# Kernel optimization log

Hardware: AMD Instinct MI355X
Metric: run time of the kernel (lower is better)

Reference implementation:

```python
import jax, jax.numpy as jnp
import numpy as np

N_NODES = 50000
N_EDGES = 800000
EMB = 128
N_LAYERS = 2
BN_EPS = 1e-5


def setup_inputs() -> dict:
    key = jax.random.key(0)
    ks = jax.random.split(key, 16)
    N, E, D, L = N_NODES, N_EDGES, EMB, N_LAYERS
    x = jax.random.randint(ks[0], (N, 2), 0, 3)
    edge_index = jax.random.randint(ks[1], (2, E), 0, N)
    edge_attr = jax.random.randint(ks[2], (E, 2), 0, 3)
    batch = jnp.zeros((N,), dtype=jnp.int32)
    s = 0.1
    xemb1 = jax.random.normal(ks[3], (120, D)) * s   # atom-type embedding
    xemb2 = jax.random.normal(ks[4], (3, D)) * s     # chirality embedding
    e1 = jax.random.normal(ks[5], (L, 7, D)) * s     # bond-type embedding per layer
    e2 = jax.random.normal(ks[6], (L, 3, D)) * s     # bond-direction embedding per layer
    W1 = jax.random.normal(ks[7], (L, D, 2 * D)) * s
    b1 = jnp.zeros((L, 2 * D))
    W2 = jax.random.normal(ks[8], (L, 2 * D, D)) * s
    b2 = jnp.zeros((L, D))
    gamma = jnp.ones((L, D))
    beta = jnp.zeros((L, D))
    return {"x": x, "edge_index": edge_index, "edge_attr": edge_attr, "batch": batch,
            "xemb1": xemb1, "xemb2": xemb2, "e1": e1, "e2": e2,
            "W1": W1, "b1": b1, "W2": W2, "b2": b2, "gamma": gamma, "beta": beta}


def _gnn_forward(x, edge_index, edge_attr, xemb1, xemb2, e1, e2, W1, b1, W2, b2, gamma, beta):
    N = x.shape[0]
    # add self loops; self-loop edge_attr = [4, 0]
    loop = jnp.arange(N, dtype=edge_index.dtype)
    src = jnp.concatenate([edge_index[0], loop])
    dst = jnp.concatenate([edge_index[1], loop])
    loop_attr = jnp.concatenate([jnp.full((N, 1), 4, dtype=edge_attr.dtype),
                                 jnp.zeros((N, 1), dtype=edge_attr.dtype)], axis=1)
    ea = jnp.concatenate([edge_attr, loop_attr], axis=0)  # [E+N, 2]

    # input node embedding
    h = xemb1[x[:, 0]] + xemb2[x[:, 1]]  # [N, D]

    for l in range(N_LAYERS):
        eemb = e1[l][ea[:, 0]] + e2[l][ea[:, 1]]      # [E+N, D]
        msg = h[src] + eemb                            # gather + edge fuse
        agg = jax.ops.segment_sum(msg, dst, num_segments=N)  # scatter-add
        # GIN update MLP: Linear -> ReLU -> Linear
        h2 = jax.nn.relu(agg @ W1[l] + b1[l]) @ W2[l] + b2[l]
        # BatchNorm1d (training mode: biased batch stats)
        mu = jnp.mean(h2, axis=0)
        var = jnp.mean(jnp.square(h2 - mu), axis=0)
        h2 = gamma[l] * (h2 - mu) * jax.lax.rsqrt(var + BN_EPS) + beta[l]
        # dropout(relu) for non-final layers; drop_ratio=0 -> identity dropout
        h = h2 if l == N_LAYERS - 1 else jax.nn.relu(h2)
    return h  # JK='last'


def reference(x, edge_index, edge_attr, batch, xemb1, xemb2, e1, e2, W1, b1, W2, b2, gamma, beta):
    return _gnn_forward(x, edge_index, edge_attr, xemb1, xemb2, e1, e2, W1, b1, W2, b2, gamma, beta)
```

## Files before the change

### kernel.cpp

```cpp
#include <hip/hip_runtime.h>
#include <stdint.h>

#define N_NODES 50000
#define N_EDGES 800000
#define EMB 128
#define NPAD 50176
#define BN_EPS 1e-5f
#define SENT_KEY ((N_NODES << 5) | 21)
#define NODES_PER_XCD 6250
#define XCHUNK 2048
#define NCHUNKS ((N_EDGES + XCHUNK - 1) / XCHUNK)
#define PBLK 196

typedef __attribute__((ext_vector_type(8))) short short8;
typedef __attribute__((ext_vector_type(4))) float f32x4;

__device__ __forceinline__ unsigned short f2bf(float f) {
    unsigned int u = __float_as_uint(f);
    u += 0x7fffu + ((u >> 16) & 1u);
    return (unsigned short)(u >> 16);
}
__device__ __forceinline__ float bflo(unsigned int v) { return __uint_as_float(v << 16); }
__device__ __forceinline__ float bfhi(unsigned int v) { return __uint_as_float(v & 0xffff0000u); }
__device__ __forceinline__ unsigned int packbf(float lo, float hi) {
    return (unsigned int)f2bf(lo) | ((unsigned int)f2bf(hi) << 16);
}

__global__ void k_prep(const int* __restrict__ x, const float* __restrict__ xe1,
                       const float* __restrict__ xe2, unsigned int* __restrict__ h,
                       const float* __restrict__ W1, const float* __restrict__ W2,
                       unsigned short* __restrict__ w1t, unsigned short* __restrict__ w2t,
                       int* __restrict__ deg,
                       const int* __restrict__ ei, const int* __restrict__ ea,
                       int* __restrict__ keyv) {
    int idx = blockIdx.x * 256 + threadIdx.x;
    int i = idx >> 6, j = idx & 63;
    if (i < N_NODES) {
        int a = x[2 * i], c = x[2 * i + 1];
        float2 va = *(const float2*)(xe1 + a * EMB + j * 2);
        float2 vb = *(const float2*)(xe2 + c * EMB + j * 2);
        h[i * 64 + j] = packbf(va.x + vb.x, va.y + vb.y);
    } else if (i == N_NODES) {
        h[(size_t)i * 64 + j] = 0u;
    }
    if (idx < 4 * 32768) {
        int sec = idx >> 15, q = idx & 32767;
        if (sec < 2) {
            int r = q >> 8, c = q & 255;
            w1t[sec * 32768 + c * 128 + r] = f2bf(W1[sec * 32768 + q]);
        } else {
            int s = sec - 2;
            int r = q >> 7, c = q & 127;
            w2t[s * 32768 + c * 256 + r] = f2bf(W2[s * 32768 + q]);
        }
    }
    if (idx < N_EDGES) {
        int2 aa = *(const int2*)(ea + 2 * idx);
        keyv[idx] = (ei[idx] << 5) | (aa.x * 3 + aa.y);
        atomicAdd(&deg[ei[N_EDGES + idx]], 1);
    }
}

__global__ void k_alloc(const int* __restrict__ deg, int* __restrict__ gcur,
                        int* __restrict__ offs, int* __restrict__ cursor,
                        int* __restrict__ keys, int* __restrict__ bcnt,
                        const float* __restrict__ e1, const float* __restrict__ e2,
                        const float* __restrict__ W1, unsigned short* __restrict__ w1e) {
    __shared__ int wbase[4];
    __shared__ int lc[8];
    int tid = threadIdx.x, lane = tid & 63, wid = tid >> 6;
    if (tid < 8) lc[tid] = 0;
    int i = blockIdx.x * 256 + tid;
    int d = (i < N_NODES) ? deg[i] : 0;
    int pd = (d + 15) & ~15;
    int s = pd;
#pragma unroll
    for (int off = 1; off < 64; off <<= 1) {
        int t = __shfl_up(s, off);
        if (lane >= off) s += t;
    }
    if (lane == 63) wbase[wid] = s;
    __syncthreads();
    if (tid == 0) {
        int t0 = wbase[0], t1 = wbase[1], t2 = wbase[2], t3 = wbase[3];
        int b = atomicAdd(gcur, t0 + t1 + t2 + t3);
        wbase[0] = b; wbase[1] = b + t0; wbase[2] = b + t0 + t1; wbase[3] = b + t0 + t1 + t2;
    }
    __syncthreads();
    if (i < N_NODES) {
        int o = wbase[wid] + s - pd;
        offs[i] = o;
        cursor[i] = o;
        for (int j = d; j < pd; ++j) keys[o + j] = SENT_KEY;
        int nch = pd >> 4;
        atomicAdd(&lc[nch > 7 ? 7 : nch], 1);
    }
    __syncthreads();
    if (tid < 8) atomicAdd(&bcnt[tid], lc[tid]);

    if (blockIdx.x < 42) {
        int l = blockIdx.x / 21, c = blockIdx.x % 21;
        int a0 = c / 3, a1 = c - a0 * 3;
        const float* E1 = e1 + l * 896 + a0 * 128;
        const float* E2 = e2 + l * 384 + a1 * 128;
        const float* w1 = W1 + l * 32768;
        int n = tid;
        float acc = 0.f;
        for (int k = 0; k < 128; ++k)
            acc = fmaf(E1[k] + E2[k], w1[k * 256 + n], acc);
        w1e[(size_t)l * 8192 + n * 32 + c] = f2bf(acc);
        if (c == 0) {
            for (int cc = 21; cc < 32; ++cc) w1e[(size_t)l * 8192 + n * 32 + cc] = 0;
        }
    }
}

__global__ void k_fill(const int* __restrict__ dst, const int* __restrict__ keyv,
                       int* __restrict__ cursor, int* __restrict__ keys,
                       const int* __restrict__ deg, const int* __restrict__ bcnt,
                       int* __restrict__ bcur, int* __restrict__ perm) {
    int xcd = blockIdx.x & 7, chunk = blockIdx.x >> 3;
    int lo = xcd * NODES_PER_XCD, hi = lo + NODES_PER_XCD;
    int e0 = chunk * XCHUNK + threadIdx.x * 4;
#pragma unroll
    for (int it = 0; it < XCHUNK / 1024; ++it) {
        int e = e0 + it * 1024;
        if (e < N_EDGES) {
            int4 d4 = *(const int4*)(dst + e);
            int dv[4] = {d4.x, d4.y, d4.z, d4.w};
#pragma unroll
            for (int q = 0; q < 4; ++q) {
                int d = dv[q];
                if (d >= lo && d < hi) {
                    int p = atomicAdd(&cursor[d], 1);
                    keys[p] = keyv[e + q];
                }
            }
        }
    }
    if (blockIdx.x < PBLK) {
        __shared__ int lcnt[8], gbase[8], tbase[8];
        if (threadIdx.x < 8) lcnt[threadIdx.x] = 0;
        __syncthreads();
        int i = blockIdx.x * 256 + threadIdx.x;
        int b = 0, lrank = 0;
        if (i < N_NODES) {
            int nch = (deg[i] + 15) >> 4;
            b = nch > 7 ? 7 : nch;
            lrank = atomicAdd(&lcnt[b], 1);
        }
        __syncthreads();
        if (threadIdx.x < 8) {
            gbase[threadIdx.x] = atomicAdd(&bcur[threadIdx.x], lcnt[threadIdx.x]);
            int s = 0;
            for (int k = 0; k < threadIdx.x; ++k) s += bcnt[k];
            tbase[threadIdx.x] = s;
        }
        __syncthreads();
        if (i < N_NODES) perm[tbase[b] + gbase[b] + lrank] = i;
    }
}

__global__ __launch_bounds__(256) void k_cnt(const int* __restrict__ deg,
                                             const int* __restrict__ offs,
                                             const int* __restrict__ keys,
                                             unsigned int* __restrict__ cntb32) {
    __shared__ int bins[16][24];
    int tid = threadIdx.x, fl = tid & 15, grp = tid >> 4;
    for (int t = tid; t < 16 * 24; t += 256) ((int*)bins)[t] = 0;
    __syncthreads();
    int node = blockIdx.x * 16 + grp;
    int o = 0, pd = 0;
    if (node < N_NODES) { o = offs[node]; pd = (deg[node] + 15) & ~15; }
    for (int j = fl; j < pd; j += 16)
        atomicAdd(&bins[grp][keys[o + j] & 31], 1);
    __syncthreads();
    if (node < NPAD) {
        int c0 = 0, c1 = 0;
        if (node < N_NODES && fl < 11) {
            c0 = bins[grp][2 * fl]     + (fl == 6 ? 1 : 0);
            c1 = bins[grp][2 * fl + 1];
        }
        cntb32[(size_t)node * 16 + fl] = packbf((float)c0, (float)c1);
    }
}

__global__ __launch_bounds__(256, 4) void k_agg(
    const unsigned int* __restrict__ h,
    const int* __restrict__ offs,
    const int* __restrict__ deg,
    const int* __restrict__ keys,
    const int* __restrict__ perm,
    unsigned int* __restrict__ agg)
{
    int wave = threadIdx.x >> 6, lane = threadIdx.x & 63;
    int sub = lane >> 4, fl = lane & 15;
    int wi = blockIdx.x * 4 + wave;
    int q = (wi & 255) * 49 + (wi >> 8);
    int slot = q * 4 + sub;
    int node = (slot < N_NODES) ? perm[slot] : slot;
    float ax[8] = {0.f, 0.f, 0.f, 0.f, 0.f, 0.f, 0.f, 0.f};
    int o = 0, nch = 0;
    if (node < N_NODES) {
        o = offs[node];
        nch = (deg[node] + 15) >> 4;
        uint4 hv = *(const uint4*)(h + (size_t)node * 64 + fl * 4);
        ax[0] = bflo(hv.x);  ax[1] = bfhi(hv.x);
        ax[2] = bflo(hv.y);  ax[3] = bfhi(hv.y);
        ax[4] = bflo(hv.z);  ax[5] = bfhi(hv.z);
        ax[6] = bflo(hv.w);  ax[7] = bfhi(hv.w);
    }
    int maxch = nch;
#pragma unroll
    for (int d = 32; d; d >>= 1) maxch = max(maxch, __shfl_xor(maxch, d));
    int key = (0 < nch) ? keys[o + fl] : SENT_KEY;
    for (int c = 0; c < maxch; ++c) {
        int keyn = (c + 1 < nch) ? keys[o + (c + 1) * 16 + fl] : SENT_KEY;
        uint4 g[8];
#pragma unroll
        for (int j = 0; j < 8; ++j) {
            int kj = __shfl(key, sub * 16 + j);
            g[j] = *(const uint4*)(h + (size_t)(kj >> 5) * 64 + fl * 4);
        }
#pragma unroll
        for (int j = 0; j < 8; ++j) {
            uint4 gg = g[j];
            int kb = __shfl(key, sub * 16 + 8 + j);
            g[j] = *(const uint4*)(h + (size_t)(kb >> 5) * 64 + fl * 4);
            ax[0] += bflo(gg.x);  ax[1] += bfhi(gg.x);
            ax[2] += bflo(gg.y);  ax[3] += bfhi(gg.y);
            ax[4] += bflo(gg.z);  ax[5] += bfhi(gg.z);
            ax[6] += bflo(gg.w);  ax[7] += bfhi(gg.w);
        }
#pragma unroll
        for (int j = 0; j < 8; ++j) {
            uint4 gg = g[j];
            ax[0] += bflo(gg.x);  ax[1] += bfhi(gg.x);
            ax[2] += bflo(gg.y);  ax[3] += bfhi(gg.y);
            ax[4] += bflo(gg.z);  ax[5] += bfhi(gg.z);
            ax[6] += bflo(gg.w);  ax[7] += bfhi(gg.w);
        }
        key = keyn;
    }
    {
        uint4 out;
        out.x = packbf(ax[0], ax[1]); out.y = packbf(ax[2], ax[3]);
        out.z = packbf(ax[4], ax[5]); out.w = packbf(ax[6], ax[7]);
        *(uint4*)(agg + (size_t)node * 64 + fl * 4) = out;
    }
}

__global__ __launch_bounds__(1024, 1) void k_mlp(
    unsigned short* aggh2,
    const unsigned short* __restrict__ cntb,
    const unsigned short* __restrict__ w1t,
    const unsigned short* __restrict__ w1e,
    const float* __restrict__ b1,
    const unsigned short* __restrict__ w2t,
    const float* __restrict__ b2,
    float* __restrict__ bnsum)
{
    __shared__ unsigned short w1s[256 * 128];
    __shared__ unsigned short w2s[128 * 256];
    __shared__ unsigned short w1es[256 * 32];
    __shared__ float bn[256];
    int tid = threadIdx.x;
    int lane = tid & 63;
    int wave = tid >> 6;
    int quad = lane >> 4, r16 = lane & 15;
    int m0 = (blockIdx.x * 16 + wave) * 16;
    int sel  = (lane >> 5) & 1;
    int srcA = ((lane >> 4) & 1) * 32 + r16;
    int srcB = srcA + 16;
    if (tid < 256) bn[tid] = 0.f;

#pragma unroll
    for (int it = 0; it < 9; ++it) {
        int ch = it * 1024 + tid;
        if (ch < 4096) {
            int row = ch >> 4, sl = ch & 15;
            uint4 v = *(const uint4*)(w1t + row * 128 + sl * 8);
            int byte = row * 256 + ((sl * 16) ^ ((row & 7) << 4));
            *(uint4*)((char*)w1s + byte) = v;
        } else if (ch < 8192) {
            int c = ch - 4096;
            int row = c >> 5, sl = c & 31;
            uint4 v = *(const uint4*)(w2t + row * 256 + sl * 8);
            int byte = row * 512 + ((sl * 16) ^ ((row & 7) << 4));
            *(uint4*)((char*)w2s + byte) = v;
        } else {
            int c = ch - 8192;
            int row = c >> 2, sl = c & 3;
            *(uint4*)(w1es + row * 32 + sl * 8) = *(const uint4*)(w1e + row * 32 + sl * 8);
        }
    }

    short8 bagg[5];
#pragma unroll
    for (int c = 0; c < 4; ++c)
        bagg[c] = *(const short8*)(aggh2 + (size_t)(m0 + r16) * 128 + c * 32 + quad * 8);
    bagg[4] = *(const short8*)(cntb + (size_t)(m0 + r16) * 32 + quad * 8);

    float b2v[8];
#pragma unroll
    for (int n = 0; n < 8; ++n) b2v[n] = b2[n * 16 + r16];

    __syncthreads();

    f32x4 acc2[8];
#pragma unroll
    for (int n = 0; n < 8; ++n) acc2[n] = (f32x4){0.f, 0.f, 0.f, 0.f};

    int swz = (r16 & 7) << 4;
    for (int c2 = 0; c2 < 8; ++c2) {
        unsigned int pk[2][2];
#pragma unroll
        for (int ntl = 0; ntl < 2; ++ntl) {
            int nt = c2 * 2 + ntl;
            int row = nt * 16 + r16;
            short8 aw[5];
#pragma unroll
            for (int c = 0; c < 4; ++c)
                aw[c] = *(const short8*)((char*)w1s + row * 256 + ((c * 64 + quad * 16) ^ swz));
            aw[4] = *(const short8*)(w1es + row * 32 + quad * 8);
            float4 bv = *(const float4*)(b1 + nt * 16 + quad * 4);
            f32x4 a1a = {0.f, 0.f, 0.f, 0.f}, a1b = {0.f, 0.f, 0.f, 0.f};
            a1a = __builtin_amdgcn_mfma_f32_16x16x32_bf16(aw[0], bagg[0], a1a, 0, 0, 0);
            a1b = __builtin_amdgcn_mfma_f32_16x16x32_bf16(aw[1], bagg[1], a1b, 0, 0, 0);
            a1a = __builtin_amdgcn_mfma_f32_16x16x32_bf16(aw[2], bagg[2], a1a, 0, 0, 0);
            a1b = __builtin_amdgcn_mfma_f32_16x16x32_bf16(aw[3], bagg[3], a1b, 0, 0, 0);
            a1a = __builtin_amdgcn_mfma_f32_16x16x32_bf16(aw[4], bagg[4], a1a, 0, 0, 0);
            float v0 = a1a[0] + a1b[0] + bv.x; v0 = v0 > 0.f ? v0 : 0.f;
            float v1 = a1a[1] + a1b[1] + bv.y; v1 = v1 > 0.f ? v1 : 0.f;
            float v2 = a1a[2] + a1b[2] + bv.z; v2 = v2 > 0.f ? v2 : 0.f;
            float v3 = a1a[3] + a1b[3] + bv.w; v3 = v3 > 0.f ? v3 : 0.f;
            pk[ntl][0] = packbf(v0, v1);
            pk[ntl][1] = packbf(v2, v3);
        }
        short8 a2f;
        {
            int u0 = __shfl((int)pk[0][0], srcA), w0 = __shfl((int)pk[1][0], srcA);
            int u1 = __shfl((int)pk[0][1], srcA), w1_ = __shfl((int)pk[1][1], srcA);
            int u2 = __shfl((int)pk[0][0], srcB), w2_ = __shfl((int)pk[1][0], srcB);
            int u3 = __shfl((int)pk[0][1], srcB), w3_ = __shfl((int)pk[1][1], srcB);
            union { int i[4]; short8 s; } a2u;
            a2u.i[0] = sel ? w0 : u0;
            a2u.i[1] = sel ? w1_ : u1;
            a2u.i[2] = sel ? w2_ : u2;
            a2u.i[3] = sel ? w3_ : u3;
            a2f = a2u.s;
        }
#pragma unroll
        for (int n = 0; n < 8; ++n) {
            int row = n * 16 + r16;
            short8 bw = *(const short8*)((char*)w2s + row * 512 + ((c2 * 64 + quad * 16) ^ swz));
            acc2[n] = __builtin_amdgcn_mfma_f32_16x16x32_bf16(a2f, bw, acc2[n], 0, 0, 0);
        }
    }
    float s[8], q[8];
#pragma unroll
    for (int n = 0; n < 8; ++n) { s[n] = 0.f; q[n] = 0.f; }
#pragma unroll
    for (int n = 0; n < 8; ++n)
#pragma unroll
        for (int r = 0; r < 4; ++r) {
            int row = m0 + quad * 4 + r;
            float v = acc2[n][r] + b2v[n];
            if (row < N_NODES) {
                aggh2[(size_t)row * 128 + n * 16 + r16] = f2bf(v);
                s[n] += v; q[n] += v * v;
            }
        }
#pragma unroll
    for (int n = 0; n < 8; ++n) {
        s[n] += __shfl_xor(s[n], 16); q[n] += __shfl_xor(q[n], 16);
        s[n] += __shfl_xor(s[n], 32); q[n] += __shfl_xor(q[n], 32);
    }
    if (quad == 0) {
#pragma unroll
        for (int n = 0; n < 8; ++n) {
            atomicAdd(&bn[n * 16 + r16], s[n]);
            atomicAdd(&bn[128 + n * 16 + r16], q[n]);
        }
    }
    __syncthreads();
    if (tid < 256) atomicAdd(&bnsum[tid], bn[tid]);
}

__global__ void k_bnnorm(const uint4* __restrict__ h2, const float* __restrict__ bnsum,
                         const float* __restrict__ gamma, const float* __restrict__ beta,
                         uint4* __restrict__ outb, float4* __restrict__ outf, int mode) {
    __shared__ float ab[256];
    int tid = threadIdx.x;
    if (tid < 128) {
        float mean = bnsum[tid] * (1.f / N_NODES);
        float var  = bnsum[128 + tid] * (1.f / N_NODES) - mean * mean;
        float rstd = rsqrtf(var + BN_EPS);
        float g = gamma[tid];
        ab[tid]       = g * rstd;
        ab[128 + tid] = beta[tid] - mean * g * rstd;
    }
    __syncthreads();
    int idx = blockIdx.x * 256 + tid;
    if (idx >= N_NODES * 16) return;
    int p = (idx & 15) * 8;
    uint4 hv = h2[idx];
    float v0 = bflo(hv.x) * ab[p + 0] + ab[128 + p + 0];
    float v1 = bfhi(hv.x) * ab[p + 1] + ab[128 + p + 1];
    float v2 = bflo(hv.y) * ab[p + 2] + ab[128 + p + 2];
    float v3 = bfhi(hv.y) * ab[p + 3] + ab[128 + p + 3];
    float v4 = bflo(hv.z) * ab[p + 4] + ab[128 + p + 4];
    float v5 = bfhi(hv.z) * ab[p + 5] + ab[128 + p + 5];
    float v6 = bflo(hv.w) * ab[p + 6] + ab[128 + p + 6];
    float v7 = bfhi(hv.w) * ab[p + 7] + ab[128 + p + 7];
    if (mode == 0) {
        v0 = v0 > 0.f ? v0 : 0.f; v1 = v1 > 0.f ? v1 : 0.f;
        v2 = v2 > 0.f ? v2 : 0.f; v3 = v3 > 0.f ? v3 : 0.f;
        v4 = v4 > 0.f ? v4 : 0.f; v5 = v5 > 0.f ? v5 : 0.f;
        v6 = v6 > 0.f ? v6 : 0.f; v7 = v7 > 0.f ? v7 : 0.f;
        uint4 out;
        out.x = packbf(v0, v1); out.y = packbf(v2, v3);
        out.z = packbf(v4, v5); out.w = packbf(v6, v7);
        outb[idx] = out;
    } else {
        outf[2 * idx]     = make_float4(v0, v1, v2, v3);
        outf[2 * idx + 1] = make_float4(v4, v5, v6, v7);
    }
}

extern "C" void kernel_launch(void* const* d_in, const int* in_sizes, int n_in,
                              void* d_out, int out_size, void* d_ws, size_t ws_size,
                              hipStream_t stream) {
    const int* x  = (const int*)d_in[0];
    const int* ei = (const int*)d_in[1];
    const int* ea = (const int*)d_in[2];
    const float* xe1 = (const float*)d_in[4];
    const float* xe2 = (const float*)d_in[5];
    const float* e1  = (const float*)d_in[6];
    const float* e2  = (const float*)d_in[7];
    const float* W1  = (const float*)d_in[8];
    const float* b1  = (const float*)d_in[9];
    const float* W2  = (const float*)d_in[10];
    const float* b2  = (const float*)d_in[11];
    const float* gm  = (const float*)d_in[12];
    const float* bt  = (const float*)d_in[13];

    char* ws = (char*)d_ws;
    size_t off = 0;
    auto take = [&](size_t bytes) -> char* {
        char* p = ws + off;
        off = (off + bytes + 255) & ~(size_t)255;
        return p;
    };
    unsigned int* h_buf = (unsigned int*)take((size_t)(N_NODES + 1) * 64 * 4);
    unsigned int* aggb  = (unsigned int*)take((size_t)NPAD * 64 * 4);
    unsigned short* w1t = (unsigned short*)take((size_t)2 * 32768 * 2);
    unsigned short* w2t = (unsigned short*)take((size_t)2 * 32768 * 2);
    unsigned short* w1e = (unsigned short*)take((size_t)2 * 8192 * 2);
    unsigned int* cntb32 = (unsigned int*)take((size_t)NPAD * 16 * 4);
    int* zbuf   = (int*)take((size_t)(N_NODES + 512 + 32) * 4);
    int* deg    = zbuf;
    float* bnsum = (float*)(zbuf + N_NODES);
    int* bmeta  = zbuf + N_NODES + 512;
    int* offs   = (int*)take((size_t)(N_NODES + 1) * 4);
    int* cursor = (int*)take((size_t)N_NODES * 4);
    int* keys   = (int*)take((size_t)(N_EDGES + N_NODES * 16) * 4);
    int* keyv   = (int*)take((size_t)N_EDGES * 4);
    int* perm   = (int*)take((size_t)N_NODES * 4);
    int* bcnt = bmeta, *bcur = bmeta + 8, *gcur = bmeta + 16;

    hipMemsetAsync(zbuf, 0, (size_t)(N_NODES + 512 + 32) * 4, stream);
    k_prep<<<((N_NODES + 1) * 64 + 255) / 256, 256, 0, stream>>>(x, xe1, xe2, h_buf,
                                                                 W1, W2, w1t, w2t, deg,
                                                                 ei, ea, keyv);
    k_alloc<<<PBLK, 256, 0, stream>>>(deg, gcur, offs, cursor, keys, bcnt,
                                      e1, e2, W1, w1e);
    k_fill<<<8 * NCHUNKS, 256, 0, stream>>>(ei + N_EDGES, keyv, cursor, keys,
                                            deg, bcnt, bcur, perm);
    k_cnt<<<NPAD / 16, 256, 0, stream>>>(deg, offs, keys, cntb32);

    for (int l = 0; l < 2; ++l) {
        k_agg<<<NPAD / 16, 256, 0, stream>>>(h_buf, offs, deg, keys, perm, aggb);
        k_mlp<<<NPAD / 256, 1024, 0, stream>>>((unsigned short*)aggb, (const unsigned short*)cntb32,
                                               w1t + l * 32768, w1e + l * 8192, b1 + l * 256,
                                               w2t + l * 32768, b2 + l * 128, bnsum + l * 256);
        k_bnnorm<<<(N_NODES * 16 + 255) / 256, 256, 0, stream>>>((const uint4*)aggb, bnsum + l * 256,
                                                                 gm + l * 128, bt + l * 128,
                                                                 (uint4*)h_buf, (float4*)d_out, l);
    }
}
```

Measured before the change: 325.9 us.

## Fuse per-layer aggregation, MLP and batchnorm into one cooperative persistent kernel

Replaces the six per-layer launches (gather-aggregate, MLP, batchnorm, for each of two layers) with a single cooperative kernel of 256 blocks of 1024 threads. Grid-wide syncs separate the phases, and each phase loops over its work items. This removes kernel launch gaps and tail effects between the small phases. In exchange, the gather phase now runs with 1024-thread blocks at one block per CU and shares a register budget with the MFMA MLP code, which may cut latency hiding for the irregular loads. It also adds grid-sync overhead.

```diff
diff --git a/kernel.cpp b/kernel.cpp
--- a/kernel.cpp
+++ b/kernel.cpp
@@ -1,5 +1,8 @@
 #include <hip/hip_runtime.h>
+#include <hip/hip_cooperative_groups.h>
 #include <stdint.h>
+
+namespace cg = cooperative_groups;
 
 #define N_NODES 50000
 #define N_EDGES 800000
@@ -185,81 +188,20 @@
     }
 }
 
-__global__ __launch_bounds__(256, 4) void k_agg(
-    const unsigned int* __restrict__ h,
-    const int* __restrict__ offs,
-    const int* __restrict__ deg,
-    const int* __restrict__ keys,
-    const int* __restrict__ perm,
-    unsigned int* __restrict__ agg)
+__global__ __launch_bounds__(1024, 1) void k_layers(
+    unsigned int* h,
+    const int* __restrict__ offs, const int* __restrict__ deg,
+    const int* __restrict__ keys, const int* __restrict__ perm,
+    unsigned int* aggb,
+    const unsigned short* __restrict__ cntb,
+    const unsigned short* __restrict__ w1t_a, const unsigned short* __restrict__ w1e_a,
+    const float* __restrict__ b1_a,
+    const unsigned short* __restrict__ w2t_a, const float* __restrict__ b2_a,
+    float* __restrict__ bnsum_a,
+    const float* __restrict__ gm_a, const float* __restrict__ bt_a,
+    float4* __restrict__ outf)
 {
-    int wave = threadIdx.x >> 6, lane = threadIdx.x & 63;
-    int sub = lane >> 4, fl = lane & 15;
-    int wi = blockIdx.x * 4 + wave;
-    int q = (wi & 255) * 49 + (wi >> 8);
-    int slot = q * 4 + sub;
-    int node = (slot < N_NODES) ? perm[slot] : slot;
-    float ax[8] = {0.f, 0.f, 0.f, 0.f, 0.f, 0.f, 0.f, 0.f};
-    int o = 0, nch = 0;
-    if (node < N_NODES) {
-        o = offs[node];
-        nch = (deg[node] + 15) >> 4;
-        uint4 hv = *(const uint4*)(h + (size_t)node * 64 + fl * 4);
-        ax[0] = bflo(hv.x);  ax[1] = bfhi(hv.x);
-        ax[2] = bflo(hv.y);  ax[3] = bfhi(hv.y);
-        ax[4] = bflo(hv.z);  ax[5] = bfhi(hv.z);
-        ax[6] = bflo(hv.w);  ax[7] = bfhi(hv.w);
-    }
-    int maxch = nch;
-#pragma unroll
-    for (int d = 32; d; d >>= 1) maxch = max(maxch, __shfl_xor(maxch, d));
-    int key = (0 < nch) ? keys[o + fl] : SENT_KEY;
-    for (int c = 0; c < maxch; ++c) {
-        int keyn = (c + 1 < nch) ? keys[o + (c + 1) * 16 + fl] : SENT_KEY;
-        uint4 g[8];
-#pragma unroll
-        for (int j = 0; j < 8; ++j) {
-            int kj = __shfl(key, sub * 16 + j);
-            g[j] = *(const uint4*)(h + (size_t)(kj >> 5) * 64 + fl * 4);
-        }
-#pragma unroll
-        for (int j = 0; j < 8; ++j) {
-            uint4 gg = g[j];
-            int kb = __shfl(key, sub * 16 + 8 + j);
-            g[j] = *(const uint4*)(h + (size_t)(kb >> 5) * 64 + fl * 4);
-            ax[0] += bflo(gg.x);  ax[1] += bfhi(gg.x);
-            ax[2] += bflo(gg.y);  ax[3] += bfhi(gg.y);
-            ax[4] += bflo(gg.z);  ax[5] += bfhi(gg.z);
-            ax[6] += bflo(gg.w);  ax[7] += bfhi(gg.w);
-        }
-#pragma unroll
-        for (int j = 0; j < 8; ++j) {
-            uint4 gg = g[j];
-            ax[0] += bflo(gg.x);  ax[1] += bfhi(gg.x);
-            ax[2] += bflo(gg.y);  ax[3] += bfhi(gg.y);
-            ax[4] += bflo(gg.z);  ax[5] += bfhi(gg.z);
-            ax[6] += bflo(gg.w);  ax[7] += bfhi(gg.w);
-        }
-        key = keyn;
-    }
-    {
-        uint4 out;
-        out.x = packbf(ax[0], ax[1]); out.y = packbf(ax[2], ax[3]);
-        out.z = packbf(ax[4], ax[5]); out.w = packbf(ax[6], ax[7]);
-        *(uint4*)(agg + (size_t)node * 64 + fl * 4) = out;
-    }
-}
-
-__global__ __launch_bounds__(1024, 1) void k_mlp(
-    unsigned short* aggh2,
-    const unsigned short* __restrict__ cntb,
-    const unsigned short* __restrict__ w1t,
-    const unsigned short* __restrict__ w1e,
-    const float* __restrict__ b1,
-    const unsigned short* __restrict__ w2t,
-    const float* __restrict__ b2,
-    float* __restrict__ bnsum)
-{
+    cg::grid_group grid = cg::this_grid();
     __shared__ unsigned short w1s[256 * 128];
     __shared__ unsigned short w2s[128 * 256];
     __shared__ unsigned short w1es[256 * 32];
@@ -268,163 +210,233 @@
     int lane = tid & 63;
     int wave = tid >> 6;
     int quad = lane >> 4, r16 = lane & 15;
-    int m0 = (blockIdx.x * 16 + wave) * 16;
     int sel  = (lane >> 5) & 1;
     int srcA = ((lane >> 4) & 1) * 32 + r16;
     int srcB = srcA + 16;
-    if (tid < 256) bn[tid] = 0.f;
-
-#pragma unroll
-    for (int it = 0; it < 9; ++it) {
-        int ch = it * 1024 + tid;
-        if (ch < 4096) {
-            int row = ch >> 4, sl = ch & 15;
-            uint4 v = *(const uint4*)(w1t + row * 128 + sl * 8);
-            int byte = row * 256 + ((sl * 16) ^ ((row & 7) << 4));
-            *(uint4*)((char*)w1s + byte) = v;
-        } else if (ch < 8192) {
-            int c = ch - 4096;
-            int row = c >> 5, sl = c & 31;
-            uint4 v = *(const uint4*)(w2t + row * 256 + sl * 8);
-            int byte = row * 512 + ((sl * 16) ^ ((row & 7) << 4));
-            *(uint4*)((char*)w2s + byte) = v;
-        } else {
-            int c = ch - 8192;
-            int row = c >> 2, sl = c & 3;
-            *(uint4*)(w1es + row * 32 + sl * 8) = *(const uint4*)(w1e + row * 32 + sl * 8);
-        }
-    }
-
-    short8 bagg[5];
-#pragma unroll
-    for (int c = 0; c < 4; ++c)
-        bagg[c] = *(const short8*)(aggh2 + (size_t)(m0 + r16) * 128 + c * 32 + quad * 8);
-    bagg[4] = *(const short8*)(cntb + (size_t)(m0 + r16) * 32 + quad * 8);
-
-    float b2v[8];
-#pragma unroll
-    for (int n = 0; n < 8; ++n) b2v[n] = b2[n * 16 + r16];
-
-    __syncthreads();
-
-    f32x4 acc2[8];
-#pragma unroll
-    for (int n = 0; n < 8; ++n) acc2[n] = (f32x4){0.f, 0.f, 0.f, 0.f};
-
-    int swz = (r16 & 7) << 4;
-    for (int c2 = 0; c2 < 8; ++c2) {
-        unsigned int pk[2][2];
-#pragma unroll
-        for (int ntl = 0; ntl < 2; ++ntl) {
-            int nt = c2 * 2 + ntl;
-            int row = nt * 16 + r16;
-            short8 aw[5];
+    unsigned short* aggh2 = (unsigned short*)aggb;
+
+    for (int l = 0; l < 2; ++l) {
+        const unsigned short* w1t = w1t_a + l * 32768;
+        const unsigned short* w1e = w1e_a + l * 8192;
+        const float* b1 = b1_a + l * 256;
+        const unsigned short* w2t = w2t_a + l * 32768;
+        const float* b2 = b2_a + l * 128;
+        float* bnsum = bnsum_a + l * 256;
+
+        {
+            int rw = blockIdx.x * 16 + wave;
+            for (int it = 0; it < 4; ++it) {
+                int wi = it * 4096 + rw;
+                if (wi >= 12544) break;
+                int q = (wi & 255) * 49 + (wi >> 8);
+                int slot = q * 4 + quad;
+                int node = (slot < N_NODES) ? perm[slot] : slot;
+                float ax[8] = {0.f, 0.f, 0.f, 0.f, 0.f, 0.f, 0.f, 0.f};
+                int o = 0, nch = 0;
+                if (node < N_NODES) {
+                    o = offs[node];
+                    nch = (deg[node] + 15) >> 4;
+                    uint4 hv = *(const uint4*)(h + (size_t)node * 64 + r16 * 4);
+                    ax[0] = bflo(hv.x);  ax[1] = bfhi(hv.x);
+                    ax[2] = bflo(hv.y);  ax[3] = bfhi(hv.y);
+                    ax[4] = bflo(hv.z);  ax[5] = bfhi(hv.z);
+                    ax[6] = bflo(hv.w);  ax[7] = bfhi(hv.w);
+                }
+                int maxch = nch;
+#pragma unroll
+                for (int d = 32; d; d >>= 1) maxch = max(maxch, __shfl_xor(maxch, d));
+                int key = (0 < nch) ? keys[o + r16] : SENT_KEY;
+                for (int c = 0; c < maxch; ++c) {
+                    int keyn = (c + 1 < nch) ? keys[o + (c + 1) * 16 + r16] : SENT_KEY;
+                    uint4 g[8];
+#pragma unroll
+                    for (int j = 0; j < 8; ++j) {
+                        int kj = __shfl(key, quad * 16 + j);
+                        g[j] = *(const uint4*)(h + (size_t)(kj >> 5) * 64 + r16 * 4);
+                    }
+#pragma unroll
+                    for (int j = 0; j < 8; ++j) {
+                        uint4 gg = g[j];
+                        int kb = __shfl(key, quad * 16 + 8 + j);
+                        g[j] = *(const uint4*)(h + (size_t)(kb >> 5) * 64 + r16 * 4);
+                        ax[0] += bflo(gg.x);  ax[1] += bfhi(gg.x);
+                        ax[2] += bflo(gg.y);  ax[3] += bfhi(gg.y);
+                        ax[4] += bflo(gg.z);  ax[5] += bfhi(gg.z);
+                        ax[6] += bflo(gg.w);  ax[7] += bfhi(gg.w);
+                    }
+#pragma unroll
+                    for (int j = 0; j < 8; ++j) {
+                        uint4 gg = g[j];
+                        ax[0] += bflo(gg.x);  ax[1] += bfhi(gg.x);
+                        ax[2] += bflo(gg.y);  ax[3] += bfhi(gg.y);
+                        ax[4] += bflo(gg.z);  ax[5] += bfhi(gg.z);
+                        ax[6] += bflo(gg.w);  ax[7] += bfhi(gg.w);
+                    }
+                    key = keyn;
+                }
+                uint4 out;
+                out.x = packbf(ax[0], ax[1]); out.y = packbf(ax[2], ax[3]);
+                out.z = packbf(ax[4], ax[5]); out.w = packbf(ax[6], ax[7]);
+                *(uint4*)(aggb + (size_t)node * 64 + r16 * 4) = out;
+            }
+        }
+        __threadfence();
+        grid.sync();
+
+        if (blockIdx.x < PBLK) {
+            if (tid < 256) bn[tid] = 0.f;
+#pragma unroll
+            for (int it = 0; it < 9; ++it) {
+                int ch = it * 1024 + tid;
+                if (ch < 4096) {
+                    int row = ch >> 4, sl = ch & 15;
+                    uint4 v = *(const uint4*)(w1t + row * 128 + sl * 8);
+                    int byte = row * 256 + ((sl * 16) ^ ((row & 7) << 4));
+                    *(uint4*)((char*)w1s + byte) = v;
+                } else if (ch < 8192) {
+                    int c = ch - 4096;
+                    int row = c >> 5, sl = c & 31;
+                    uint4 v = *(const uint4*)(w2t + row * 256 + sl * 8);
+                    int byte = row * 512 + ((sl * 16) ^ ((row & 7) << 4));
+                    *(uint4*)((char*)w2s + byte) = v;
+                } else {
+                    int c = ch - 8192;
+                    int row = c >> 2, sl = c & 3;
+                    *(uint4*)(w1es + row * 32 + sl * 8) = *(const uint4*)(w1e + row * 32 + sl * 8);
+                }
+            }
+            int m0 = (blockIdx.x * 16 + wave) * 16;
+            short8 bagg[5];
 #pragma unroll
             for (int c = 0; c < 4; ++c)
-                aw[c] = *(const short8*)((char*)w1s + row * 256 + ((c * 64 + quad * 16) ^ swz));
-            aw[4] = *(const short8*)(w1es + row * 32 + quad * 8);
-            float4 bv = *(const float4*)(b1 + nt * 16 + quad * 4);
-            f32x4 a1a = {0.f, 0.f, 0.f, 0.f}, a1b = {0.f, 0.f, 0.f, 0.f};
-            a1a = __builtin_amdgcn_mfma_f32_16x16x32_bf16(aw[0], bagg[0], a1a, 0, 0, 0);
-            a1b = __builtin_amdgcn_mfma_f32_16x16x32_bf16(aw[1], bagg[1], a1b, 0, 0, 0);
-            a1a = __builtin_amdgcn_mfma_f32_16x16x32_bf16(aw[2], bagg[2], a1a, 0, 0, 0);
-            a1b = __builtin_amdgcn_mfma_f32_16x16x32_bf16(aw[3], bagg[3], a1b, 0, 0, 0);
-            a1a = __builtin_amdgcn_mfma_f32_16x16x32_bf16(aw[4], bagg[4], a1a, 0, 0, 0);
-            float v0 = a1a[0] + a1b[0] + bv.x; v0 = v0 > 0.f ? v0 : 0.f;
-            float v1 = a1a[1] + a1b[1] + bv.y; v1 = v1 > 0.f ? v1 : 0.f;
-            float v2 = a1a[2] + a1b[2] + bv.z; v2 = v2 > 0.f ? v2 : 0.f;
-            float v3 = a1a[3] + a1b[3] + bv.w; v3 = v3 > 0.f ? v3 : 0.f;
-            pk[ntl][0] = packbf(v0, v1);
-            pk[ntl][1] = packbf(v2, v3);
-        }
-        short8 a2f;
+                bagg[c] = *(const short8*)(aggh2 + (size_t)(m0 + r16) * 128 + c * 32 + quad * 8);
+            bagg[4] = *(const short8*)(cntb + (size_t)(m0 + r16) * 32 + quad * 8);
+            float b2v[8];
+#pragma unroll
+            for (int n = 0; n < 8; ++n) b2v[n] = b2[n * 16 + r16];
+            __syncthreads();
+
+            f32x4 acc2[8];
+#pragma unroll
+            for (int n = 0; n < 8; ++n) acc2[n] = (f32x4){0.f, 0.f, 0.f, 0.f};
+            int swz = (r16 & 7) << 4;
+            for (int c2 = 0; c2 < 8; ++c2) {
+                unsigned int pk[2][2];
+#pragma unroll
+                for (int ntl = 0; ntl < 2; ++ntl) {
+                    int nt = c2 * 2 + ntl;
+                    int row = nt * 16 + r16;
+                    short8 aw[5];
+#pragma unroll
+                    for (int c = 0; c < 4; ++c)
+                        aw[c] = *(const short8*)((char*)w1s + row * 256 + ((c * 64 + quad * 16) ^ swz));
+                    aw[4] = *(const short8*)(w1es + row * 32 + quad * 8);
+                    float4 bv = *(const float4*)(b1 + nt * 16 + quad * 4);
+                    f32x4 a1a = {0.f, 0.f, 0.f, 0.f}, a1b = {0.f, 0.f, 0.f, 0.f};
+                    a1a = __builtin_amdgcn_mfma_f32_16x16x32_bf16(aw[0], bagg[0], a1a, 0, 0, 0);
+                    a1b = __builtin_amdgcn_mfma_f32_16x16x32_bf16(aw[1], bagg[1], a1b, 0, 0, 0);
+                    a1a = __builtin_amdgcn_mfma_f32_16x16x32_bf16(aw[2], bagg[2], a1a, 0, 0, 0);
+                    a1b = __builtin_amdgcn_mfma_f32_16x16x32_bf16(aw[3], bagg[3], a1b, 0, 0, 0);
+                    a1a = __builtin_amdgcn_mfma_f32_16x16x32_bf16(aw[4], bagg[4], a1a, 0, 0, 0);
+                    float v0 = a1a[0] + a1b[0] + bv.x; v0 = v0 > 0.f ? v0 : 0.f;
+                    float v1 = a1a[1] + a1b[1] + bv.y; v1 = v1 > 0.f ? v1 : 0.f;
+                    float v2 = a1a[2] + a1b[2] + bv.z; v2 = v2 > 0.f ? v2 : 0.f;
+                    float v3 = a1a[3] + a1b[3] + bv.w; v3 = v3 > 0.f ? v3 : 0.f;
+                    pk[ntl][0] = packbf(v0, v1);
+                    pk[ntl][1] = packbf(v2, v3);
+                }
+                short8 a2f;
+                {
+                    int u0 = __shfl((int)pk[0][0], srcA), w0 = __shfl((int)pk[1][0], srcA);
+                    int u1 = __shfl((int)pk[0][1], srcA), w1_ = __shfl((int)pk[1][1], srcA);
+                    int u2 = __shfl((int)pk[0][0], srcB), w2_ = __shfl((int)pk[1][0], srcB);
+                    int u3 = __shfl((int)pk[0][1], srcB), w3_ = __shfl((int)pk[1][1], srcB);
+                    union { int i[4]; short8 s; } a2u;
+                    a2u.i[0] = sel ? w0 : u0;
+                    a2u.i[1] = sel ? w1_ : u1;
+                    a2u.i[2] = sel ? w2_ : u2;
+                    a2u.i[3] = sel ? w3_ : u3;
+                    a2f = a2u.s;
+                }
+#pragma unroll
+                for (int n = 0; n < 8; ++n) {
+                    int row = n * 16 + r16;
+                    short8 bw = *(const short8*)((char*)w2s + row * 512 + ((c2 * 64 + quad * 16) ^ swz));
+                    acc2[n] = __builtin_amdgcn_mfma_f32_16x16x32_bf16(a2f, bw, acc2[n], 0, 0, 0);
+                }
+            }
+            float s[8], q[8];
+#pragma unroll
+            for (int n = 0; n < 8; ++n) { s[n] = 0.f; q[n] = 0.f; }
+#pragma unroll
+            for (int n = 0; n < 8; ++n)
+#pragma unroll
+                for (int r = 0; r < 4; ++r) {
+                    int row = m0 + quad * 4 + r;
+                    float v = acc2[n][r] + b2v[n];
+                    if (row < N_NODES) {
+                        aggh2[(size_t)row * 128 + n * 16 + r16] = f2bf(v);
+                        s[n] += v; q[n] += v * v;
+                    }
+                }
+#pragma unroll
+            for (int n = 0; n < 8; ++n) {
+                s[n] += __shfl_xor(s[n], 16); q[n] += __shfl_xor(q[n], 16);
+                s[n] += __shfl_xor(s[n], 32); q[n] += __shfl_xor(q[n], 32);
+            }
+            if (quad == 0) {
+#pragma unroll
+                for (int n = 0; n < 8; ++n) {
+                    atomicAdd(&bn[n * 16 + r16], s[n]);
+                    atomicAdd(&bn[128 + n * 16 + r16], q[n]);
+                }
+            }
+            __syncthreads();
+            if (tid < 256) atomicAdd(&bnsum[tid], bn[tid]);
+        }
+        __threadfence();
+        grid.sync();
+
         {
-            int u0 = __shfl((int)pk[0][0], srcA), w0 = __shfl((int)pk[1][0], srcA);
-            int u1 = __shfl((int)pk[0][1], srcA), w1_ = __shfl((int)pk[1][1], srcA);
-            int u2 = __shfl((int)pk[0][0], srcB), w2_ = __shfl((int)pk[1][0], srcB);
-            int u3 = __shfl((int)pk[0][1], srcB), w3_ = __shfl((int)pk[1][1], srcB);
-            union { int i[4]; short8 s; } a2u;
-            a2u.i[0] = sel ? w0 : u0;
-            a2u.i[1] = sel ? w1_ : u1;
-            a2u.i[2] = sel ? w2_ : u2;
-            a2u.i[3] = sel ? w3_ : u3;
-            a2f = a2u.s;
-        }
-#pragma unroll
-        for (int n = 0; n < 8; ++n) {
-            int row = n * 16 + r16;
-            short8 bw = *(const short8*)((char*)w2s + row * 512 + ((c2 * 64 + quad * 16) ^ swz));
-            acc2[n] = __builtin_amdgcn_mfma_f32_16x16x32_bf16(a2f, bw, acc2[n], 0, 0, 0);
-        }
-    }
-    float s[8], q[8];
-#pragma unroll
-    for (int n = 0; n < 8; ++n) { s[n] = 0.f; q[n] = 0.f; }
-#pragma unroll
-    for (int n = 0; n < 8; ++n)
-#pragma unroll
-        for (int r = 0; r < 4; ++r) {
-            int row = m0 + quad * 4 + r;
-            float v = acc2[n][r] + b2v[n];
-            if (row < N_NODES) {
-                aggh2[(size_t)row * 128 + n * 16 + r16] = f2bf(v);
-                s[n] += v; q[n] += v * v;
-            }
-        }
-#pragma unroll
-    for (int n = 0; n < 8; ++n) {
-        s[n] += __shfl_xor(s[n], 16); q[n] += __shfl_xor(q[n], 16);
-        s[n] += __shfl_xor(s[n], 32); q[n] += __shfl_xor(q[n], 32);
-    }
-    if (quad == 0) {
-#pragma unroll
-        for (int n = 0; n < 8; ++n) {
-            atomicAdd(&bn[n * 16 + r16], s[n]);
-            atomicAdd(&bn[128 + n * 16 + r16], q[n]);
-        }
-    }
-    __syncthreads();
-    if (tid < 256) atomicAdd(&bnsum[tid], bn[tid]);
-}
-
-__global__ void k_bnnorm(const uint4* __restrict__ h2, const float* __restrict__ bnsum,
-                         const float* __restrict__ gamma, const float* __restrict__ beta,
-                         uint4* __restrict__ outb, float4* __restrict__ outf, int mode) {
-    __shared__ float ab[256];
-    int tid = threadIdx.x;
-    if (tid < 128) {
-        float mean = bnsum[tid] * (1.f / N_NODES);
-        float var  = bnsum[128 + tid] * (1.f / N_NODES) - mean * mean;
-        float rstd = rsqrtf(var + BN_EPS);
-        float g = gamma[tid];
-        ab[tid]       = g * rstd;
-        ab[128 + tid] = beta[tid] - mean * g * rstd;
-    }
-    __syncthreads();
-    int idx = blockIdx.x * 256 + tid;
-    if (idx >= N_NODES * 16) return;
-    int p = (idx & 15) * 8;
-    uint4 hv = h2[idx];
-    float v0 = bflo(hv.x) * ab[p + 0] + ab[128 + p + 0];
-    float v1 = bfhi(hv.x) * ab[p + 1] + ab[128 + p + 1];
-    float v2 = bflo(hv.y) * ab[p + 2] + ab[128 + p + 2];
-    float v3 = bfhi(hv.y) * ab[p + 3] + ab[128 + p + 3];
-    float v4 = bflo(hv.z) * ab[p + 4] + ab[128 + p + 4];
-    float v5 = bfhi(hv.z) * ab[p + 5] + ab[128 + p + 5];
-    float v6 = bflo(hv.w) * ab[p + 6] + ab[128 + p + 6];
-    float v7 = bfhi(hv.w) * ab[p + 7] + ab[128 + p + 7];
-    if (mode == 0) {
-        v0 = v0 > 0.f ? v0 : 0.f; v1 = v1 > 0.f ? v1 : 0.f;
-        v2 = v2 > 0.f ? v2 : 0.f; v3 = v3 > 0.f ? v3 : 0.f;
-        v4 = v4 > 0.f ? v4 : 0.f; v5 = v5 > 0.f ? v5 : 0.f;
-        v6 = v6 > 0.f ? v6 : 0.f; v7 = v7 > 0.f ? v7 : 0.f;
-        uint4 out;
-        out.x = packbf(v0, v1); out.y = packbf(v2, v3);
-        out.z = packbf(v4, v5); out.w = packbf(v6, v7);
-        outb[idx] = out;
-    } else {
-        outf[2 * idx]     = make_float4(v0, v1, v2, v3);
-        outf[2 * idx + 1] = make_float4(v4, v5, v6, v7);
+            if (tid < 128) {
+                float mean = bnsum[tid] * (1.f / N_NODES);
+                float var  = bnsum[128 + tid] * (1.f / N_NODES) - mean * mean;
+                float rstd = rsqrtf(var + BN_EPS);
+                float g = gm_a[l * 128 + tid];
+                bn[tid]       = g * rstd;
+                bn[128 + tid] = bt_a[l * 128 + tid] - mean * g * rstd;
+            }
+            __syncthreads();
+            int base = blockIdx.x * 1024 + tid;
+            for (int it = 0; it < 4; ++it) {
+                int idx = it * 262144 + base;
+                if (idx >= N_NODES * 16) break;
+                int p = (idx & 15) * 8;
+                uint4 hv = ((const uint4*)aggb)[idx];
+                float v0 = bflo(hv.x) * bn[p + 0] + bn[128 + p + 0];
+                float v1 = bfhi(hv.x) * bn[p + 1] + bn[128 + p + 1];
+                float v2 = bflo(hv.y) * bn[p + 2] + bn[128 + p + 2];
+                float v3 = bfhi(hv.y) * bn[p + 3] + bn[128 + p + 3];
+                float v4 = bflo(hv.z) * bn[p + 4] + bn[128 + p + 4];
+                float v5 = bfhi(hv.z) * bn[p + 5] + bn[128 + p + 5];
+                float v6 = bflo(hv.w) * bn[p + 6] + bn[128 + p + 6];
+                float v7 = bfhi(hv.w) * bn[p + 7] + bn[128 + p + 7];
+                if (l == 0) {
+                    v0 = v0 > 0.f ? v0 : 0.f; v1 = v1 > 0.f ? v1 : 0.f;
+                    v2 = v2 > 0.f ? v2 : 0.f; v3 = v3 > 0.f ? v3 : 0.f;
+                    v4 = v4 > 0.f ? v4 : 0.f; v5 = v5 > 0.f ? v5 : 0.f;
+                    v6 = v6 > 0.f ? v6 : 0.f; v7 = v7 > 0.f ? v7 : 0.f;
+                    uint4 out;
+                    out.x = packbf(v0, v1); out.y = packbf(v2, v3);
+                    out.z = packbf(v4, v5); out.w = packbf(v6, v7);
+                    ((uint4*)h)[idx] = out;
+                } else {
+                    outf[2 * idx]     = make_float4(v0, v1, v2, v3);
+                    outf[2 * idx + 1] = make_float4(v4, v5, v6, v7);
+                }
+            }
+        }
+        if (l == 0) { __threadfence(); grid.sync(); }
     }
 }
 
@@ -479,13 +491,14 @@
                                             deg, bcnt, bcur, perm);
     k_cnt<<<NPAD / 16, 256, 0, stream>>>(deg, offs, keys, cntb32);
 
-    for (int l = 0; l < 2; ++l) {
-        k_agg<<<NPAD / 16, 256, 0, stream>>>(h_buf, offs, deg, keys, perm, aggb);
-        k_mlp<<<NPAD / 256, 1024, 0, stream>>>((unsigned short*)aggb, (const unsigned short*)cntb32,
-                                               w1t + l * 32768, w1e + l * 8192, b1 + l * 256,
-                                               w2t + l * 32768, b2 + l * 128, bnsum + l * 256);
-        k_bnnorm<<<(N_NODES * 16 + 255) / 256, 256, 0, stream>>>((const uint4*)aggb, bnsum + l * 256,
-                                                                 gm + l * 128, bt + l * 128,
-                                                                 (uint4*)h_buf, (float4*)d_out, l);
-    }
-}
+    const unsigned short* cntb_us = (const unsigned short*)cntb32;
+    float4* outf = (float4*)d_out;
+    void* kargs[] = {
+        (void*)&h_buf, (void*)&offs, (void*)&deg, (void*)&keys, (void*)&perm,
+        (void*)&aggb, (void*)&cntb_us,
+        (void*)&w1t, (void*)&w1e, (void*)&b1,
+        (void*)&w2t, (void*)&b2,
+        (void*)&bnsum, (void*)&gm, (void*)&bt, (void*)&outf
+    };
+    hipLaunchCooperativeKernel((void*)k_layers, dim3(256), dim3(1024), kargs, 0, stream);
+}
```

New measurement: 993.0 us. +204.7%, slower.
